# Kernel optimization log

Measured on AMD Instinct MI355X. Metric: run time of the kernel, lower is better.

Reference implementation:

```python
import jax, jax.numpy as jnp
import numpy as np

KS = 3
N = KS ** 3  # 27 kernel taps
EPS = 1e-5

def conv3d(x, w, stride=1, padding=0):
    return jax.lax.conv_general_dilated(
        x, w, (stride,) * 3, [(padding, padding)] * 3,
        dimension_numbers=('NCDHW', 'OIDHW', 'NCDHW'))

def batchnorm(x, gamma, beta):
    mu = jnp.mean(x, axis=(0, 2, 3, 4), keepdims=True)
    var = jnp.var(x, axis=(0, 2, 3, 4), keepdims=True)
    return (x - mu) * jax.lax.rsqrt(var + EPS) * gamma[None, :, None, None, None] + beta[None, :, None, None, None]

def deform_conv3d(x, w_p, b_p, w_m, b_m, w_dc):
    b, c, D, H, W = x.shape
    offset = conv3d(x, w_p, padding=1) + b_p[None, :, None, None, None]      # (b,3N,D,H,W)
    m = jax.nn.sigmoid(conv3d(x, w_m, padding=1) + b_m[None, :, None, None, None])  # (b,N,D,H,W)
    x_pad = jnp.pad(x, ((0, 0), (0, 0), (1, 1), (1, 1), (1, 1)))
    Dp, Hp, Wp = D + 2, H + 2, W + 2
    r = jnp.arange(-(KS - 1) // 2, KS // 2 + 1, dtype=x.dtype)
    pn_d, pn_h, pn_w = [a.reshape(-1) for a in jnp.meshgrid(r, r, r, indexing='ij')]
    off = offset.transpose(0, 2, 3, 4, 1)                                    # (b,D,H,W,3N)
    p0_d = jnp.arange(1, D + 1, dtype=x.dtype)[:, None, None, None]
    p0_h = jnp.arange(1, H + 1, dtype=x.dtype)[None, :, None, None]
    p0_w = jnp.arange(1, W + 1, dtype=x.dtype)[None, None, :, None]
    pd = p0_d + pn_d + off[..., :N]
    ph = p0_h + pn_h + off[..., N:2 * N]
    pw = p0_w + pn_w + off[..., 2 * N:]
    d0 = jnp.clip(jnp.floor(pd), 0.0, Dp - 1.0); d1 = jnp.clip(d0 + 1.0, 0.0, Dp - 1.0)
    h0 = jnp.clip(jnp.floor(ph), 0.0, Hp - 1.0); h1 = jnp.clip(h0 + 1.0, 0.0, Hp - 1.0)
    w0 = jnp.clip(jnp.floor(pw), 0.0, Wp - 1.0); w1 = jnp.clip(w0 + 1.0, 0.0, Wp - 1.0)
    pd = jnp.clip(pd, 0.0, Dp - 1.0); ph = jnp.clip(ph, 0.0, Hp - 1.0); pw = jnp.clip(pw, 0.0, Wp - 1.0)
    xf = x_pad.reshape(b, c, -1)
    def gather(qd, qh, qw):
        idx = (qd * (Hp * Wp) + qh * Wp + qw).astype(jnp.int32).reshape(b, 1, -1)
        v = jnp.take_along_axis(xf, jnp.broadcast_to(idx, (b, c, idx.shape[-1])), axis=2)
        return v.reshape(b, c, D, H, W, N)
    x_off = jnp.zeros((b, c, D, H, W, N), x.dtype)
    for qd, wd in ((d0, 1.0 + d0 - pd), (d1, 1.0 - d1 + pd)):
        for qh, wh in ((h0, 1.0 + h0 - ph), (h1, 1.0 - h1 + ph)):
            for qw, ww in ((w0, 1.0 + w0 - pw), (w1, 1.0 - w1 + pw)):
                x_off = x_off + (wd * wh * ww)[:, None] * gather(qd, qh, qw)
    x_off = x_off * m.transpose(0, 2, 3, 4, 1)[:, None]                      # modulation
    # interleave kernel taps: (b,c,D,kd,H,kh,W,kw) -> (b,c,D*KS,H*KS,W*KS)
    x_off = x_off.reshape(b, c, D, H, W, KS, KS, KS)
    x_off = x_off.transpose(0, 1, 2, 5, 3, 6, 4, 7).reshape(b, c, D * KS, H * KS, W * KS)
    out = conv3d(x_off, w_dc, stride=KS)
    p = jnp.concatenate([pd, ph, pw], axis=-1)                               # (b,D,H,W,3N)
    return out, p

def setup_inputs() -> dict:
    key = jax.random.key(0)
    ks = jax.random.split(key, 10)
    B, D = 4, 48
    return {
        'x': jax.random.normal(ks[0], (B, 1, D, D, D), jnp.float32),
        'w_p': jax.random.normal(ks[1], (3 * N, 1, KS, KS, KS), jnp.float32) * 0.05,
        'b_p': jnp.zeros((3 * N,), jnp.float32),
        'w_m': jax.random.normal(ks[2], (N, 1, KS, KS, KS), jnp.float32) * 0.1,
        'b_m': jnp.zeros((N,), jnp.float32),
        'w_dc': jax.random.normal(ks[3], (1, 1, KS, KS, KS), jnp.float32) * 0.2,
        'g_d': jnp.ones((1,), jnp.float32), 'be_d': jnp.zeros((1,), jnp.float32),
        'w_c1': jax.random.normal(ks[4], (32, 1, KS, KS, KS), jnp.float32) * 0.3,
        'g1': jnp.ones((32,), jnp.float32), 'be1': jnp.zeros((32,), jnp.float32),
        'w_c2': jax.random.normal(ks[5], (64, 32, KS, KS, KS), jnp.float32) * 0.06,
        'g2': jnp.ones((64,), jnp.float32), 'be2': jnp.zeros((64,), jnp.float32),
        'w_fc': jax.random.normal(ks[6], (10, 64), jnp.float32) * 0.1,
        'b_fc': jnp.zeros((10,), jnp.float32),
    }

def reference(x, w_p, b_p, w_m, b_m, w_dc, g_d, be_d, w_c1, g1, be1, w_c2, g2, be2, w_fc, b_fc):
    inp = x
    for _ in range(2):
        y, p = deform_conv3d(inp, w_p, b_p, w_m, b_m, w_dc)
        xxx = y
        inp = jax.nn.relu(batchnorm(y, g_d, be_d))
    h = jax.nn.relu(batchnorm(conv3d(inp, w_c1, padding=1), g1, be1))
    h = jax.nn.relu(batchnorm(conv3d(h, w_c2, padding=1), g2, be2))
    h = jax.lax.reduce_window(h, -jnp.inf, jax.lax.max, (1, 1, 3, 3, 3), (1, 1, 3, 3, 3), 'VALID')
    h = h.mean(axis=(2, 3, 4))                       # adaptive avg pool to 1
    logits = h @ w_fc.T + b_fc
    return logits, xxx, p
```

## Files before the change

### kernel.cpp

```cpp
#include <hip/hip_runtime.h>
#include <math.h>

#define BSZ 4
#define DD 48
#define SS (48*48*48)
#define NV (BSZ*SS)
#define PS 125000
#define EPSBN 1e-5f

typedef __attribute__((ext_vector_type(8))) short bf16x8;
typedef __attribute__((ext_vector_type(4))) short s16x4;
typedef __attribute__((ext_vector_type(4))) float f32x4;

__device__ __forceinline__ short f2b(float f){
  unsigned u = __float_as_uint(f);
  u = (u + 0x7FFFu + ((u>>16)&1u)) >> 16;
  return (short)u;
}
__device__ __forceinline__ float b2f(short s){
  return __uint_as_float(((unsigned)(unsigned short)s)<<16);
}

__global__ __launch_bounds__(256) void pad_kernel(
    const float* __restrict__ src, float* __restrict__ dst)
{
  int idx = blockIdx.x*256 + threadIdx.x;
  if (idx >= BSZ*PS) return;
  int b = idx / PS; int r = idx - b*PS;
  int z = r/2500; int r2 = r - z*2500; int yy = r2/50; int xx = r2 - yy*50;
  float v = 0.f;
  if (z>=1 && z<=48 && yy>=1 && yy<=48 && xx>=1 && xx<=48)
    v = src[(size_t)b*SS + (size_t)((z-1)*48 + (yy-1))*48 + (xx-1)];
  dst[idx] = v;
}

__global__ __launch_bounds__(256) void bnpad_kernel(
    const float* __restrict__ y, const float* __restrict__ st,
    const float* __restrict__ gamma, const float* __restrict__ beta,
    float* __restrict__ xpad)
{
  int idx = blockIdx.x*256 + threadIdx.x;
  if (idx >= BSZ*PS) return;
  float mu  = st[0]*(1.f/(float)NV);
  float var = st[1]*(1.f/(float)NV) - mu*mu;
  float sc  = rsqrtf(var+EPSBN)*gamma[0];
  float sh  = beta[0] - mu*sc;
  int b = idx / PS; int r = idx - b*PS;
  int z = r/2500; int r2 = r - z*2500; int yy = r2/50; int xx = r2 - yy*50;
  float v = 0.f;
  if (z>=1 && z<=48 && yy>=1 && yy<=48 && xx>=1 && xx<=48){
    float t = y[(size_t)b*SS + (size_t)((z-1)*48 + (yy-1))*48 + (xx-1)];
    v = fmaxf(fmaf(t, sc, sh), 0.f);
  }
  xpad[idx] = v;
}

__global__ void woff2_kernel(const float* __restrict__ w_p, const float* __restrict__ b_p,
                             const float* __restrict__ w_m, const float* __restrict__ b_m,
                             short* __restrict__ wo2)
{
  int o = blockIdx.x*256 + threadIdx.x;
  if (o >= 112*32) return;
  int k = o & 31; int c = o >> 5;
  int f = c >> 4, qq = (c >> 2) & 3, r = c & 3;
  int n = 4*f + qq;
  float v = 0.f;
  if (n < 27){
    if (k < 27)       v = (r < 3) ? w_p[(r*27+n)*27 + k] : w_m[n*27 + k];
    else if (k == 27) v = (r < 3) ? b_p[r*27+n]          : b_m[n];
  }
  wo2[o] = f2b(v);
}

__global__ void wconv1_kernel(const float* __restrict__ w, short* __restrict__ wb)
{
  int o = blockIdx.x*256 + threadIdx.x;
  if (o >= 32*32) return;
  int k = o & 31; int c = o >> 5;
  wb[o] = f2b(k < 27 ? w[c*27 + k] : 0.f);
}

template<bool WRITE_P>
__global__ __launch_bounds__(256) void deform3_kernel(
    const float* __restrict__ xpad,
    const short* __restrict__ wo2,
    const float* __restrict__ w_dc,
    float* __restrict__ y, float* __restrict__ p_out,
    float* __restrict__ st)
{
  __shared__ short xt[6*6*18];
  __shared__ __align__(16) float pbuf[WRITE_P ? 64*81 : 4];
  __shared__ float yred[8];

  int bid = blockIdx.x;
  int bw = bid % 3; int bh = (bid/3)%12; int bd = (bid/36)%12; int b = bid/432;
  int d0 = bd*4, h0 = bh*4, w0 = bw*16;
  int tid = threadIdx.x;
  const float* xp = xpad + (size_t)b*PS;

  for (int e = tid; e < 648; e += 256){
    int z = e/108; int rem = e - z*108; int yy = rem/18; int xx = rem - yy*18;
    xt[e] = f2b(xp[(d0+z)*2500 + (h0+yy)*50 + (w0+xx)]);
  }
  __syncthreads();

  int lane = tid & 63, wid = tid >> 6;
  int q = lane >> 4, n16 = lane & 15;

  bf16x8 aF[7];
  #pragma unroll
  for (int f=0; f<7; ++f)
    aF[f] = *(const bf16x8*)(wo2 + (f*16 + n16)*32 + q*8);

  int toffs[8];
  #pragma unroll
  for (int j=0;j<8;++j){
    int t = q*8 + j; int tc = t > 26 ? 0 : t;
    int kd = tc/9, rr = tc - kd*9, kh = rr/3, kw = rr - kh*3;
    toffs[j] = kd*108 + kh*18 + kw;
  }

  float wdcv[7], fkd[7], fkh[7], fkw[7];
  #pragma unroll
  for (int f=0; f<7; ++f){
    int n = 4*f + q;
    if (n < 27){
      int kd = n/9, rr = n - kd*9, kh = rr/3, kw = rr - kh*3;
      wdcv[f] = w_dc[n];
      fkd[f] = (float)kd; fkh[f] = (float)kh; fkw[f] = (float)kw;
    } else { wdcv[f]=0.f; fkd[f]=0.f; fkh[f]=0.f; fkw[f]=0.f; }
  }

  const short one_bf = (short)0x3F80;
  const f32x4 zero4 = {0.f,0.f,0.f,0.f};
  float based = (float)(d0 + wid);
  float basew = (float)(w0 + n16);
  float ys = 0.f, yq = 0.f;

  #pragma unroll 1
  for (int dy=0; dy<4; ++dy){
    int vbase = wid*108 + dy*18 + n16;
    bf16x8 bF;
    #pragma unroll
    for (int j=0;j<8;++j){
      short xv = xt[vbase + toffs[j]];
      bF[j] = (j<3 || q<3) ? xv : one_bf;
    }
    f32x4 acc[7];
    #pragma unroll
    for (int f=0; f<7; ++f)
      acc[f] = __builtin_amdgcn_mfma_f32_16x16x32_bf16(aF[f], bF, zero4, 0,0,0);

    float baseh = (float)(h0 + dy);
    float accv = 0.f;
    #pragma unroll
    for (int f=0; f<7; ++f){
      int n = 4*f + q;
      if (n < 27){
        float od = acc[f][0], oh = acc[f][1], ow = acc[f][2], mr = acc[f][3];
        float mm = __builtin_amdgcn_rcpf(1.f + __expf(-mr));
        float pdv = based + fkd[f] + od;
        float phv = baseh + fkh[f] + oh;
        float pwv = basew + fkw[f] + ow;
        float fd0 = fminf(fmaxf(floorf(pdv),0.f),49.f), fd1 = fminf(fd0+1.f,49.f);
        float pdc = fminf(fmaxf(pdv,0.f),49.f);
        float wd0 = 1.f + fd0 - pdc, wd1 = 1.f - fd1 + pdc;
        float fh0 = fminf(fmaxf(floorf(phv),0.f),49.f), fh1 = fminf(fh0+1.f,49.f);
        float phc = fminf(fmaxf(phv,0.f),49.f);
        float wh0 = 1.f + fh0 - phc, wh1 = 1.f - fh1 + phc;
        float fw0 = fminf(fmaxf(floorf(pwv),0.f),49.f), fw1 = fminf(fw0+1.f,49.f);
        float pwc = fminf(fmaxf(pwv,0.f),49.f);
        float wwa = 1.f + fw0 - pwc, wwb = 1.f - fw1 + pwc;
        int iz0 = (int)fd0*2500, iz1 = (int)fd1*2500;
        int iy0 = (int)fh0*50,   iy1 = (int)fh1*50;
        int ix0 = (int)fw0,      ix1 = (int)fw1;
        float v000=xp[iz0+iy0+ix0], v001=xp[iz0+iy0+ix1];
        float v010=xp[iz0+iy1+ix0], v011=xp[iz0+iy1+ix1];
        float v100=xp[iz1+iy0+ix0], v101=xp[iz1+iy0+ix1];
        float v110=xp[iz1+iy1+ix0], v111=xp[iz1+iy1+ix1];
        float sv = wd0*(wh0*(wwa*v000+wwb*v001)+wh1*(wwa*v010+wwb*v011))
                 + wd1*(wh0*(wwa*v100+wwb*v101)+wh1*(wwa*v110+wwb*v111));
        accv += sv*mm*wdcv[f];
        if constexpr (WRITE_P){
          int vb = (wid*16 + n16)*81;
          pbuf[vb + n]      = pdc;
          pbuf[vb + 27 + n] = phc;
          pbuf[vb + 54 + n] = pwc;
        }
      }
    }
    accv += __shfl_xor(accv, 16);
    accv += __shfl_xor(accv, 32);
    if (q == 0){
      y[(size_t)b*SS + (size_t)((d0+wid)*48 + (h0+dy))*48 + (w0+n16)] = accv;
      ys += accv; yq += accv*accv;
    }

    if constexpr (WRITE_P){
      __syncthreads();
      size_t rbase = ((((size_t)b*48 + (d0+wid))*48 + (h0+dy))*48 + w0)*81;
      const float* src = pbuf + wid*1296;
      float* dst = p_out + rbase;
      #pragma unroll
      for (int k=0;k<6;++k){
        int i4 = (lane + (k<<6))<<2;
        if (i4 < 1296){
          f32x4 v = *(const f32x4*)(src + i4);
          *(f32x4*)(dst + i4) = v;
        }
      }
      __syncthreads();
    }
  }

  ys += __shfl_xor(ys, 1); ys += __shfl_xor(ys, 2);
  ys += __shfl_xor(ys, 4); ys += __shfl_xor(ys, 8);
  yq += __shfl_xor(yq, 1); yq += __shfl_xor(yq, 2);
  yq += __shfl_xor(yq, 4); yq += __shfl_xor(yq, 8);
  if (lane == 0){ yred[wid] = ys; yred[4+wid] = yq; }
  __syncthreads();
  if (tid == 0) atomicAdd(&st[0], yred[0]+yred[1]+yred[2]+yred[3]);
  if (tid == 1) atomicAdd(&st[1], yred[4]+yred[5]+yred[6]+yred[7]);
}

__global__ __launch_bounds__(256) void conv1m_kernel(
    const float* __restrict__ xpad, const short* __restrict__ wc1b,
    short* __restrict__ h1c)
{
  __shared__ short xt[6*6*18];
  int bid = blockIdx.x;
  int bw = bid % 3; int bh = (bid/3)%12; int bd = (bid/36)%12; int b = bid/432;
  int d0 = bd*4, h0 = bh*4, w0 = bw*16;
  int tid = threadIdx.x;
  const float* xp = xpad + (size_t)b*PS;

  for (int e = tid; e < 648; e += 256){
    int z = e/108; int rem = e - z*108; int yy = rem/18; int xx = rem - yy*18;
    xt[e] = f2b(xp[(d0+z)*2500 + (h0+yy)*50 + (w0+xx)]);
  }
  __syncthreads();

  int lane = tid & 63, wid = tid >> 6;
  int q = lane >> 4, n16 = lane & 15;

  bf16x8 aF0 = *(const bf16x8*)(wc1b + n16*32 + q*8);
  bf16x8 aF1 = *(const bf16x8*)(wc1b + (16+n16)*32 + q*8);

  int toffs[8];
  #pragma unroll
  for (int j=0;j<8;++j){
    int t = q*8 + j; int tc = t > 26 ? 0 : t;
    int kd = tc/9, rr = tc - kd*9, kh = rr/3, kw = rr - kh*3;
    toffs[j] = kd*108 + kh*18 + kw;
  }

  const f32x4 zero4 = {0.f,0.f,0.f,0.f};
  #pragma unroll
  for (int dy=0; dy<4; ++dy){
    int vbase = wid*108 + dy*18 + n16;
    bf16x8 bF;
    #pragma unroll
    for (int j=0;j<8;++j) bF[j] = xt[vbase + toffs[j]];
    f32x4 a0 = __builtin_amdgcn_mfma_f32_16x16x32_bf16(aF0, bF, zero4, 0,0,0);
    f32x4 a1 = __builtin_amdgcn_mfma_f32_16x16x32_bf16(aF1, bF, zero4, 0,0,0);
    size_t idx = (size_t)b*SS + (size_t)((d0+wid)*48 + (h0+dy))*48 + (w0+n16);
    s16x4 o0, o1;
    #pragma unroll
    for (int r=0;r<4;++r){ o0[r]=f2b(a0[r]); o1[r]=f2b(a1[r]); }
    *(s16x4*)(h1c + idx*32 + q*4)      = o0;
    *(s16x4*)(h1c + idx*32 + 16 + q*4) = o1;
  }
}

template<int NCH>
__global__ __launch_bounds__(256) void bn_stats_cl(
    const short* __restrict__ x, float* __restrict__ sums)
{
  constexpr int GPB = NCH/8;
  const long NG = (long)NV*GPB;
  int tid = threadIdx.x;
  f32x4 sa = {0.f,0.f,0.f,0.f}, sb = sa, qa = sa, qb = sa;
  for (long g = (long)blockIdx.x*256+tid; g < NG; g += (long)gridDim.x*256){
    bf16x8 v8 = *(const bf16x8*)(x + g*8);
    float v;
    v=b2f(v8[0]); sa[0]+=v; qa[0]+=v*v;
    v=b2f(v8[1]); sa[1]+=v; qa[1]+=v*v;
    v=b2f(v8[2]); sa[2]+=v; qa[2]+=v*v;
    v=b2f(v8[3]); sa[3]+=v; qa[3]+=v*v;
    v=b2f(v8[4]); sb[0]+=v; qb[0]+=v*v;
    v=b2f(v8[5]); sb[1]+=v; qb[1]+=v*v;
    v=b2f(v8[6]); sb[2]+=v; qb[2]+=v*v;
    v=b2f(v8[7]); sb[3]+=v; qb[3]+=v*v;
  }
  #pragma unroll
  for (int m = GPB; m < 64; m <<= 1){
    sa[0]+=__shfl_xor(sa[0],m); sa[1]+=__shfl_xor(sa[1],m);
    sa[2]+=__shfl_xor(sa[2],m); sa[3]+=__shfl_xor(sa[3],m);
    sb[0]+=__shfl_xor(sb[0],m); sb[1]+=__shfl_xor(sb[1],m);
    sb[2]+=__shfl_xor(sb[2],m); sb[3]+=__shfl_xor(sb[3],m);
    qa[0]+=__shfl_xor(qa[0],m); qa[1]+=__shfl_xor(qa[1],m);
    qa[2]+=__shfl_xor(qa[2],m); qa[3]+=__shfl_xor(qa[3],m);
    qb[0]+=__shfl_xor(qb[0],m); qb[1]+=__shfl_xor(qb[1],m);
    qb[2]+=__shfl_xor(qb[2],m); qb[3]+=__shfl_xor(qb[3],m);
  }
  int lane = tid & 63, wid = tid >> 6;
  __shared__ float red[4][GPB][16];
  if (lane < GPB){
    red[wid][lane][0]=sa[0];  red[wid][lane][1]=sa[1];
    red[wid][lane][2]=sa[2];  red[wid][lane][3]=sa[3];
    red[wid][lane][4]=sb[0];  red[wid][lane][5]=sb[1];
    red[wid][lane][6]=sb[2];  red[wid][lane][7]=sb[3];
    red[wid][lane][8]=qa[0];  red[wid][lane][9]=qa[1];
    red[wid][lane][10]=qa[2]; red[wid][lane][11]=qa[3];
    red[wid][lane][12]=qb[0]; red[wid][lane][13]=qb[1];
    red[wid][lane][14]=qb[2]; red[wid][lane][15]=qb[3];
  }
  __syncthreads();
  if (tid < GPB*16){
    int gi = tid >> 4, v = tid & 15;
    float t = red[0][gi][v] + red[1][gi][v] + red[2][gi][v] + red[3][gi][v];
    int ch = gi*8 + (v & 7);
    atomicAdd(&sums[2*ch + (v>>3)], t);
  }
}

__global__ __launch_bounds__(256) void conv2_mfma2(
    const short* __restrict__ h1c, const short* __restrict__ wbf,
    const float* __restrict__ st1, const float* __restrict__ g1,
    const float* __restrict__ be1, short* __restrict__ t2c)
{
  __shared__ __align__(16) short slab[4*648*8];
  __shared__ float ssc[32], ssh[32];
  int tid = threadIdx.x;
  if (tid < 32){
    float mu  = st1[2*tid]  *(1.f/(float)NV);
    float var = st1[2*tid+1]*(1.f/(float)NV) - mu*mu;
    float sc = rsqrtf(var+EPSBN)*g1[tid];
    ssc[tid]=sc; ssh[tid]=be1[tid]-mu*sc;
  }
  __syncthreads();

  int bid0 = blockIdx.x;
  int bid = (bid0 & 7)*216 + (bid0 >> 3);
  int bw = bid % 3; int bh = (bid/3)%12; int bd = (bid/36)%12; int b = bid/432;
  int d0 = bd*4, h0 = bh*4, w0 = bw*16;
  const short* hb = h1c + (size_t)b*SS*32;

  for (int e = tid; e < 648; e += 256){
    int z = e/108; int rem = e - z*108; int y = rem/18; int x = rem - y*18;
    int gd = d0-1+z, gh = h0-1+y, gw = w0-1+x;
    bool ok = ((unsigned)gd<48u)&&((unsigned)gh<48u)&&((unsigned)gw<48u);
    if (ok){
      const bf16x8* src = (const bf16x8*)(hb + (size_t)((gd*48+gh)*48+gw)*32);
      #pragma unroll
      for (int g8=0; g8<4; ++g8){
        bf16x8 raw = src[g8];
        bf16x8 outv;
        #pragma unroll
        for (int j=0;j<8;++j){
          float v = fmaxf(fmaf(b2f(raw[j]), ssc[g8*8+j], ssh[g8*8+j]), 0.f);
          outv[j] = f2b(v);
        }
        *(bf16x8*)&slab[(g8*648+e)*8] = outv;
      }
    } else {
      bf16x8 zz = {0,0,0,0,0,0,0,0};
      #pragma unroll
      for (int g8=0; g8<4; ++g8) *(bf16x8*)&slab[(g8*648+e)*8] = zz;
    }
  }
  __syncthreads();

  int lane = tid & 63, wid = tid >> 6;
  int q = lane >> 4, n16 = lane & 15;
  f32x4 zero4 = {0.f,0.f,0.f,0.f};
  f32x4 acc[4][4];
  #pragma unroll
  for (int i=0;i<4;++i)
  #pragma unroll
  for (int j=0;j<4;++j) acc[i][j] = zero4;

  #pragma unroll 1
  for (int tap=0; tap<27; ++tap){
    int kd = tap/9; int kh = (tap/3)%3; int kw = tap%3;
    const short* wp = wbf + (size_t)tap*64*32 + n16*32 + q*8;
    bf16x8 aF[4];
    #pragma unroll
    for (int mb=0; mb<4; ++mb)
      aF[mb] = *(const bf16x8*)(wp + mb*16*32);

    int zz = wid + kd;
    #pragma unroll
    for (int dy=0; dy<4; ++dy){
      int e = (zz*6 + (dy+kh))*18 + (n16+kw);
      bf16x8 bF = *(const bf16x8*)&slab[(q*648 + e)*8];
      #pragma unroll
      for (int mb=0; mb<4; ++mb)
        acc[mb][dy] = __builtin_amdgcn_mfma_f32_16x16x32_bf16(aF[mb], bF, acc[mb][dy], 0,0,0);
    }
  }

  short* tb = t2c + (size_t)b*SS*64;
  #pragma unroll
  for (int dy=0; dy<4; ++dy){
    int svox = ((d0+wid)*48 + (h0+dy))*48 + (w0+n16);
    #pragma unroll
    for (int mb=0; mb<4; ++mb){
      s16x4 o4;
      #pragma unroll
      for (int r=0;r<4;++r) o4[r] = f2b(acc[mb][dy][r]);
      *(s16x4*)(tb + (size_t)svox*64 + mb*16 + q*4) = o4;
    }
  }
}

__global__ void wconv_kernel(const float* __restrict__ w, short* __restrict__ wbf)
{
  int o = blockIdx.x*blockDim.x + threadIdx.x;
  if (o >= 27*64*32) return;
  int ci = o & 31; int co = (o>>5) & 63; int tap = o >> 11;
  wbf[o] = f2b(w[(co*32+ci)*27 + tap]);
}

__global__ __launch_bounds__(128) void pool64c_kernel(
    const short* __restrict__ t2c, const float* __restrict__ sums,
    const float* __restrict__ gamma, const float* __restrict__ beta,
    float* __restrict__ pooled)
{
  __shared__ float ssc[64], ssh[64];
  int tid = threadIdx.x;
  if (tid < 64){
    float mu  = sums[2*tid]  *(1.f/(float)NV);
    float var = sums[2*tid+1]*(1.f/(float)NV) - mu*mu;
    float sc = rsqrtf(var+EPSBN)*gamma[tid];
    ssc[tid]=sc; ssh[tid]=beta[tid]-mu*sc;
  }
  __syncthreads();
  int b = blockIdx.z, pd = blockIdx.y, ph = blockIdx.x;
  int c8 = tid & 7, pw = tid >> 3;
  const short* tb = t2c + (size_t)b*SS*64;
  f32x4 mxa = {-1e30f,-1e30f,-1e30f,-1e30f}, mxb = mxa;
  float sc0=ssc[c8*8+0], sc1=ssc[c8*8+1], sc2=ssc[c8*8+2], sc3=ssc[c8*8+3];
  float sc4=ssc[c8*8+4], sc5=ssc[c8*8+5], sc6=ssc[c8*8+6], sc7=ssc[c8*8+7];
  float sh0=ssh[c8*8+0], sh1=ssh[c8*8+1], sh2=ssh[c8*8+2], sh3=ssh[c8*8+3];
  float sh4=ssh[c8*8+4], sh5=ssh[c8*8+5], sh6=ssh[c8*8+6], sh7=ssh[c8*8+7];
  #pragma unroll
  for (int kd=0;kd<3;++kd)
  #pragma unroll 1
  for (int kh=0;kh<3;++kh)
  #pragma unroll
  for (int kw=0;kw<3;++kw){
    int vox = ((pd*3+kd)*48 + (ph*3+kh))*48 + (pw*3+kw);
    bf16x8 v8 = *(const bf16x8*)(tb + (size_t)vox*64 + c8*8);
    float v;
    v = fmaxf(fmaf(b2f(v8[0]), sc0, sh0), 0.f); mxa[0] = fmaxf(mxa[0], v);
    v = fmaxf(fmaf(b2f(v8[1]), sc1, sh1), 0.f); mxa[1] = fmaxf(mxa[1], v);
    v = fmaxf(fmaf(b2f(v8[2]), sc2, sh2), 0.f); mxa[2] = fmaxf(mxa[2], v);
    v = fmaxf(fmaf(b2f(v8[3]), sc3, sh3), 0.f); mxa[3] = fmaxf(mxa[3], v);
    v = fmaxf(fmaf(b2f(v8[4]), sc4, sh4), 0.f); mxb[0] = fmaxf(mxb[0], v);
    v = fmaxf(fmaf(b2f(v8[5]), sc5, sh5), 0.f); mxb[1] = fmaxf(mxb[1], v);
    v = fmaxf(fmaf(b2f(v8[6]), sc6, sh6), 0.f); mxb[2] = fmaxf(mxb[2], v);
    v = fmaxf(fmaf(b2f(v8[7]), sc7, sh7), 0.f); mxb[3] = fmaxf(mxb[3], v);
  }
  __shared__ float r[128][8];
  r[tid][0]=mxa[0]; r[tid][1]=mxa[1]; r[tid][2]=mxa[2]; r[tid][3]=mxa[3];
  r[tid][4]=mxb[0]; r[tid][5]=mxb[1]; r[tid][6]=mxb[2]; r[tid][7]=mxb[3];
  __syncthreads();
  for (int o=64;o>=8;o>>=1){
    if (tid<o){
      #pragma unroll
      for (int j=0;j<8;++j) r[tid][j]+=r[tid+o][j];
    }
    __syncthreads();
  }
  if (tid<8){
    #pragma unroll
    for (int j=0;j<8;++j) atomicAdd(&pooled[b*64 + tid*8 + j], r[tid][j]);
  }
}

__global__ void fc_kernel(const float* __restrict__ pooled,
                          const float* __restrict__ w_fc, const float* __restrict__ b_fc,
                          float* __restrict__ logits)
{
  int t = threadIdx.x;
  if (t < 40){
    int b = t/10, k = t - 10*(t/10);
    float a = b_fc[k];
    #pragma unroll 1
    for (int c=0;c<64;++c) a = fmaf(pooled[b*64+c]*(1.f/4096.f), w_fc[k*64+c], a);
    logits[b*10+k] = a;
  }
}

extern "C" void kernel_launch(void* const* d_in, const int* in_sizes, int n_in,
                              void* d_out, int out_size, void* d_ws, size_t ws_size,
                              hipStream_t stream)
{
  const float* x    = (const float*)d_in[0];
  const float* w_p  = (const float*)d_in[1];
  const float* b_p  = (const float*)d_in[2];
  const float* w_m  = (const float*)d_in[3];
  const float* b_m  = (const float*)d_in[4];
  const float* w_dc = (const float*)d_in[5];
  const float* g_d  = (const float*)d_in[6];
  const float* be_d = (const float*)d_in[7];
  const float* w_c1 = (const float*)d_in[8];
  const float* g1   = (const float*)d_in[9];
  const float* be1  = (const float*)d_in[10];
  const float* w_c2 = (const float*)d_in[11];
  const float* g2   = (const float*)d_in[12];
  const float* be2  = (const float*)d_in[13];
  const float* w_fc = (const float*)d_in[14];
  const float* b_fc = (const float*)d_in[15];

  float* out    = (float*)d_out;
  float* logits = out;
  float* xxx    = out + 40;
  float* p_out  = out + 40 + NV;

  float* ws     = (float*)d_ws;
  float* stats  = ws;
  float* pooled = stats + 512;
  short* wbf    = (short*)(pooled + 256);
  short* wo2    = wbf + 27*64*32;
  short* wc1b   = wo2 + 112*32;
  float* xpad   = (float*)(wc1b + 32*32);
  float* y1     = xpad + (size_t)BSZ*PS;
  short* h1c    = (short*)(y1 + NV);
  short* t2c    = h1c + (size_t)NV*32;

  float* st_y1 = stats + 0;
  float* st_y2 = stats + 2;
  float* st_h1 = stats + 4;
  float* st_t2 = stats + 68;

  const int pblk = (BSZ*PS + 255)/256;

  hipMemsetAsync(stats, 0, (512+256)*sizeof(float), stream);

  wconv_kernel<<<(27*64*32+255)/256,256,0,stream>>>(w_c2, wbf);
  woff2_kernel<<<(112*32+255)/256,256,0,stream>>>(w_p, b_p, w_m, b_m, wo2);
  wconv1_kernel<<<(32*32+255)/256,256,0,stream>>>(w_c1, wc1b);

  pad_kernel<<<pblk,256,0,stream>>>(x, xpad);
  deform3_kernel<false><<<1728,256,0,stream>>>(xpad, wo2, w_dc, y1, nullptr, st_y1);
  bnpad_kernel<<<pblk,256,0,stream>>>(y1, st_y1, g_d, be_d, xpad);

  deform3_kernel<true><<<1728,256,0,stream>>>(xpad, wo2, w_dc, xxx, p_out, st_y2);
  bnpad_kernel<<<pblk,256,0,stream>>>(xxx, st_y2, g_d, be_d, xpad);

  conv1m_kernel<<<1728,256,0,stream>>>(xpad, wc1b, h1c);
  bn_stats_cl<32><<<256,256,0,stream>>>(h1c, st_h1);

  conv2_mfma2<<<1728,256,0,stream>>>(h1c, wbf, st_h1, g1, be1, t2c);
  bn_stats_cl<64><<<512,256,0,stream>>>(t2c, st_t2);
  pool64c_kernel<<<dim3(16,16,BSZ),128,0,stream>>>(t2c, st_t2, g2, be2, pooled);

  fc_kernel<<<1,64,0,stream>>>(pooled, w_fc, b_fc, logits);
}
```

Before: 374.6 us.

## Store padded volume as packed bf16 x-pairs to halve trilinear gathers

The padded input volume is now stored as packed bf16 pairs (element x and x+1) in one 32-bit word. The deform kernel's trilinear sampling then needs four loads instead of eight, and the smem tile loads skip the float-to-bf16 conversion. The WRITE_P path also drops its two block-wide barriers, since each wave writes and reads only its own slice of the staging buffer. In exchange, the sampled values are rounded to bf16, which lowers accuracy compared with fp32 gathers.

```diff
diff --git a/kernel.cpp b/kernel.cpp
--- a/kernel.cpp
+++ b/kernel.cpp
@@ -21,23 +21,29 @@
   return __uint_as_float(((unsigned)(unsigned short)s)<<16);
 }
 
-__global__ __launch_bounds__(256) void pad_kernel(
-    const float* __restrict__ src, float* __restrict__ dst)
+__global__ __launch_bounds__(256) void pad_pair_kernel(
+    const float* __restrict__ src, unsigned* __restrict__ dst)
 {
   int idx = blockIdx.x*256 + threadIdx.x;
   if (idx >= BSZ*PS) return;
   int b = idx / PS; int r = idx - b*PS;
   int z = r/2500; int r2 = r - z*2500; int yy = r2/50; int xx = r2 - yy*50;
-  float v = 0.f;
-  if (z>=1 && z<=48 && yy>=1 && yy<=48 && xx>=1 && xx<=48)
-    v = src[(size_t)b*SS + (size_t)((z-1)*48 + (yy-1))*48 + (xx-1)];
-  dst[idx] = v;
-}
-
-__global__ __launch_bounds__(256) void bnpad_kernel(
+  const float* sb = src + (size_t)b*SS;
+  auto val = [&](int zz,int yv,int xv)->unsigned{
+    float v = 0.f;
+    if (zz>=1 && zz<=48 && yv>=1 && yv<=48 && xv>=1 && xv<=48)
+      v = sb[(size_t)((zz-1)*48 + (yv-1))*48 + (xv-1)];
+    return (unsigned)(unsigned short)f2b(v);
+  };
+  unsigned lo = val(z,yy,xx);
+  unsigned hi = (xx<49) ? val(z,yy,xx+1) : 0u;
+  dst[idx] = lo | (hi<<16);
+}
+
+__global__ __launch_bounds__(256) void bnpad_pair_kernel(
     const float* __restrict__ y, const float* __restrict__ st,
     const float* __restrict__ gamma, const float* __restrict__ beta,
-    float* __restrict__ xpad)
+    unsigned* __restrict__ dst)
 {
   int idx = blockIdx.x*256 + threadIdx.x;
   if (idx >= BSZ*PS) return;
@@ -47,12 +53,18 @@
   float sh  = beta[0] - mu*sc;
   int b = idx / PS; int r = idx - b*PS;
   int z = r/2500; int r2 = r - z*2500; int yy = r2/50; int xx = r2 - yy*50;
-  float v = 0.f;
-  if (z>=1 && z<=48 && yy>=1 && yy<=48 && xx>=1 && xx<=48){
-    float t = y[(size_t)b*SS + (size_t)((z-1)*48 + (yy-1))*48 + (xx-1)];
-    v = fmaxf(fmaf(t, sc, sh), 0.f);
-  }
-  xpad[idx] = v;
+  const float* yb = y + (size_t)b*SS;
+  auto val = [&](int zz,int yv,int xv)->unsigned{
+    float v = 0.f;
+    if (zz>=1 && zz<=48 && yv>=1 && yv<=48 && xv>=1 && xv<=48){
+      float t = yb[(size_t)((zz-1)*48 + (yv-1))*48 + (xv-1)];
+      v = fmaxf(fmaf(t, sc, sh), 0.f);
+    }
+    return (unsigned)(unsigned short)f2b(v);
+  };
+  unsigned lo = val(z,yy,xx);
+  unsigned hi = (xx<49) ? val(z,yy,xx+1) : 0u;
+  dst[idx] = lo | (hi<<16);
 }
 
 __global__ void woff2_kernel(const float* __restrict__ w_p, const float* __restrict__ b_p,
@@ -82,25 +94,25 @@
 
 template<bool WRITE_P>
 __global__ __launch_bounds__(256) void deform3_kernel(
-    const float* __restrict__ xpad,
+    const unsigned* __restrict__ xpair,
     const short* __restrict__ wo2,
     const float* __restrict__ w_dc,
     float* __restrict__ y, float* __restrict__ p_out,
     float* __restrict__ st)
 {
   __shared__ short xt[6*6*18];
-  __shared__ __align__(16) float pbuf[WRITE_P ? 64*81 : 4];
+  __shared__ __align__(16) float pbuf[WRITE_P ? 4*16*81 : 4];
   __shared__ float yred[8];
 
   int bid = blockIdx.x;
   int bw = bid % 3; int bh = (bid/3)%12; int bd = (bid/36)%12; int b = bid/432;
   int d0 = bd*4, h0 = bh*4, w0 = bw*16;
   int tid = threadIdx.x;
-  const float* xp = xpad + (size_t)b*PS;
+  const unsigned* xp = xpair + (size_t)b*PS;
 
   for (int e = tid; e < 648; e += 256){
     int z = e/108; int rem = e - z*108; int yy = rem/18; int xx = rem - yy*18;
-    xt[e] = f2b(xp[(d0+z)*2500 + (h0+yy)*50 + (w0+xx)]);
+    xt[e] = (short)(xp[(d0+z)*2500 + (h0+yy)*50 + (w0+xx)] & 0xffffu);
   }
   __syncthreads();
 
@@ -136,6 +148,7 @@
   float based = (float)(d0 + wid);
   float basew = (float)(w0 + n16);
   float ys = 0.f, yq = 0.f;
+  float* pw = pbuf + wid*1296;
 
   #pragma unroll 1
   for (int dy=0; dy<4; ++dy){
@@ -168,24 +181,33 @@
         float fh0 = fminf(fmaxf(floorf(phv),0.f),49.f), fh1 = fminf(fh0+1.f,49.f);
         float phc = fminf(fmaxf(phv,0.f),49.f);
         float wh0 = 1.f + fh0 - phc, wh1 = 1.f - fh1 + phc;
-        float fw0 = fminf(fmaxf(floorf(pwv),0.f),49.f), fw1 = fminf(fw0+1.f,49.f);
+        float fw0 = fminf(fmaxf(floorf(pwv),0.f),49.f);
         float pwc = fminf(fmaxf(pwv,0.f),49.f);
+        float fw1 = fminf(fw0+1.f,49.f);
         float wwa = 1.f + fw0 - pwc, wwb = 1.f - fw1 + pwc;
         int iz0 = (int)fd0*2500, iz1 = (int)fd1*2500;
         int iy0 = (int)fh0*50,   iy1 = (int)fh1*50;
-        int ix0 = (int)fw0,      ix1 = (int)fw1;
-        float v000=xp[iz0+iy0+ix0], v001=xp[iz0+iy0+ix1];
-        float v010=xp[iz0+iy1+ix0], v011=xp[iz0+iy1+ix1];
-        float v100=xp[iz1+iy0+ix0], v101=xp[iz1+iy0+ix1];
-        float v110=xp[iz1+iy1+ix0], v111=xp[iz1+iy1+ix1];
+        int ix0 = (int)fw0;
+        bool sel = ix0 > 48;
+        int ixp = sel ? 48 : ix0;
+        unsigned p00 = xp[iz0+iy0+ixp], p01 = xp[iz0+iy1+ixp];
+        unsigned p10 = xp[iz1+iy0+ixp], p11 = xp[iz1+iy1+ixp];
+        float lo00=b2f((short)p00), hi00=b2f((short)(p00>>16));
+        float lo01=b2f((short)p01), hi01=b2f((short)(p01>>16));
+        float lo10=b2f((short)p10), hi10=b2f((short)(p10>>16));
+        float lo11=b2f((short)p11), hi11=b2f((short)(p11>>16));
+        float v000 = sel ? hi00 : lo00, v001 = hi00;
+        float v010 = sel ? hi01 : lo01, v011 = hi01;
+        float v100 = sel ? hi10 : lo10, v101 = hi10;
+        float v110 = sel ? hi11 : lo11, v111 = hi11;
         float sv = wd0*(wh0*(wwa*v000+wwb*v001)+wh1*(wwa*v010+wwb*v011))
                  + wd1*(wh0*(wwa*v100+wwb*v101)+wh1*(wwa*v110+wwb*v111));
         accv += sv*mm*wdcv[f];
         if constexpr (WRITE_P){
-          int vb = (wid*16 + n16)*81;
-          pbuf[vb + n]      = pdc;
-          pbuf[vb + 27 + n] = phc;
-          pbuf[vb + 54 + n] = pwc;
+          int vb = n16*81;
+          pw[vb + n]      = pdc;
+          pw[vb + 27 + n] = phc;
+          pw[vb + 54 + n] = pwc;
         }
       }
     }
@@ -197,19 +219,16 @@
     }
 
     if constexpr (WRITE_P){
-      __syncthreads();
       size_t rbase = ((((size_t)b*48 + (d0+wid))*48 + (h0+dy))*48 + w0)*81;
-      const float* src = pbuf + wid*1296;
       float* dst = p_out + rbase;
       #pragma unroll
       for (int k=0;k<6;++k){
-        int i4 = (lane + (k<<6))<<2;
-        if (i4 < 1296){
-          f32x4 v = *(const f32x4*)(src + i4);
-          *(f32x4*)(dst + i4) = v;
+        int i = lane + (k<<6);
+        if (i < 324){
+          f32x4 v = *(const f32x4*)(pw + i*4);
+          *(f32x4*)(dst + i*4) = v;
         }
       }
-      __syncthreads();
     }
   }
 
@@ -224,7 +243,7 @@
 }
 
 __global__ __launch_bounds__(256) void conv1m_kernel(
-    const float* __restrict__ xpad, const short* __restrict__ wc1b,
+    const unsigned* __restrict__ xpair, const short* __restrict__ wc1b,
     short* __restrict__ h1c)
 {
   __shared__ short xt[6*6*18];
@@ -232,11 +251,11 @@
   int bw = bid % 3; int bh = (bid/3)%12; int bd = (bid/36)%12; int b = bid/432;
   int d0 = bd*4, h0 = bh*4, w0 = bw*16;
   int tid = threadIdx.x;
-  const float* xp = xpad + (size_t)b*PS;
+  const unsigned* xp = xpair + (size_t)b*PS;
 
   for (int e = tid; e < 648; e += 256){
     int z = e/108; int rem = e - z*108; int yy = rem/18; int xx = rem - yy*18;
-    xt[e] = f2b(xp[(d0+z)*2500 + (h0+yy)*50 + (w0+xx)]);
+    xt[e] = (short)(xp[(d0+z)*2500 + (h0+yy)*50 + (w0+xx)] & 0xffffu);
   }
   __syncthreads();
 
@@ -525,8 +544,8 @@
   short* wbf    = (short*)(pooled + 256);
   short* wo2    = wbf + 27*64*32;
   short* wc1b   = wo2 + 112*32;
-  float* xpad   = (float*)(wc1b + 32*32);
-  float* y1     = xpad + (size_t)BSZ*PS;
+  unsigned* xpair = (unsigned*)(wc1b + 32*32);
+  float* y1     = (float*)(xpair + (size_t)BSZ*PS);
   short* h1c    = (short*)(y1 + NV);
   short* t2c    = h1c + (size_t)NV*32;
 
@@ -543,14 +562,14 @@
   woff2_kernel<<<(112*32+255)/256,256,0,stream>>>(w_p, b_p, w_m, b_m, wo2);
   wconv1_kernel<<<(32*32+255)/256,256,0,stream>>>(w_c1, wc1b);
 
-  pad_kernel<<<pblk,256,0,stream>>>(x, xpad);
-  deform3_kernel<false><<<1728,256,0,stream>>>(xpad, wo2, w_dc, y1, nullptr, st_y1);
-  bnpad_kernel<<<pblk,256,0,stream>>>(y1, st_y1, g_d, be_d, xpad);
-
-  deform3_kernel<true><<<1728,256,0,stream>>>(xpad, wo2, w_dc, xxx, p_out, st_y2);
-  bnpad_kernel<<<pblk,256,0,stream>>>(xxx, st_y2, g_d, be_d, xpad);
-
-  conv1m_kernel<<<1728,256,0,stream>>>(xpad, wc1b, h1c);
+  pad_pair_kernel<<<pblk,256,0,stream>>>(x, xpair);
+  deform3_kernel<false><<<1728,256,0,stream>>>(xpair, wo2, w_dc, y1, nullptr, st_y1);
+  bnpad_pair_kernel<<<pblk,256,0,stream>>>(y1, st_y1, g_d, be_d, xpair);
+
+  deform3_kernel<true><<<1728,256,0,stream>>>(xpair, wo2, w_dc, xxx, p_out, st_y2);
+  bnpad_pair_kernel<<<pblk,256,0,stream>>>(xxx, st_y2, g_d, be_d, xpair);
+
+  conv1m_kernel<<<1728,256,0,stream>>>(xpair, wc1b, h1c);
   bn_stats_cl<32><<<256,256,0,stream>>>(h1c, st_h1);
 
   conv2_mfma2<<<1728,256,0,stream>>>(h1c, wbf, st_h1, g1, be1, t2c);
```

Measured after the change: 342.0 us. 1.1x faster.
